# Kernel tuning notes

Measured on AMD Instinct MI355X. Metric: run time of the kernel, lower is better.

## Reference

```python
import jax, jax.numpy as jnp
import numpy as np

MUL = 64  # multiplicity of 0e and 1o in each input (irreps: 64x0e + 64x1o)
SQRT3 = float(np.sqrt(3.0))
SQRT2 = float(np.sqrt(2.0))
# Levi-Civita tensor: wigner_3j(1,1,1) is eps/sqrt(6); with 'component' norm it is scaled by sqrt(3) -> eps/sqrt(2)
_EPS = np.zeros((3, 3, 3), dtype=np.float32)
_EPS[0, 1, 2] = _EPS[1, 2, 0] = _EPS[2, 0, 1] = 1.0
_EPS[0, 2, 1] = _EPS[2, 1, 0] = _EPS[1, 0, 2] = -1.0
EPS = jnp.asarray(_EPS)


def setup_inputs() -> dict:
    key = jax.random.key(0)
    k1, k2 = jax.random.split(key)
    N = 4096
    D = MUL * (1 + 3)  # 64 scalars (0e) + 64 vectors (1o) = 256
    return {
        "input1": jax.random.normal(k1, (N, D), dtype=jnp.float32),
        "input2": jax.random.normal(k2, (N, D), dtype=jnp.float32),
    }


def _full_tensor_product(input1, input2):
    lead = input1.shape[:-1]
    a0 = input1[..., :MUL]                            # (..., 64)    0e chunk
    a1 = input1[..., MUL:].reshape(lead + (MUL, 3))   # (..., 64, 3) 1o chunk
    b0 = input2[..., :MUL]
    b1 = input2[..., MUL:].reshape(lead + (MUL, 3))
    # 'component' normalization: cg *= sqrt(dim(ir_out))
    # path 0e x 0e -> 0e : cg = 1
    c_000 = jnp.einsum('...u,...v->...uv', a0, b0).reshape(lead + (MUL * MUL,))
    # path 1o x 1o -> 0e : cg = eye(3)/sqrt(3)  (normalized dot product)
    c_110 = (jnp.einsum('...ui,...vi->...uv', a1, b1) / SQRT3).reshape(lead + (MUL * MUL,))
    # path 0e x 1o -> 1o : cg = eye(3)  (eye/sqrt3 * sqrt3)
    c_011 = jnp.einsum('...u,...vj->...uvj', a0, b1).reshape(lead + (MUL * MUL * 3,))
    # path 1o x 0e -> 1o : cg = eye(3)
    c_101 = jnp.einsum('...ui,...v->...uvi', a1, b0).reshape(lead + (MUL * MUL * 3,))
    # path 1o x 1o -> 1e : cg = eps/sqrt(2)  (normalized cross product)
    c_111 = jnp.einsum('...ui,...vj,ijk->...uvk', a1, b1, EPS / SQRT2).reshape(lead + (MUL * MUL * 3,))
    # sorted output irreps: 4096x0e + 4096x0e + 4096x1o + 4096x1o + 4096x1e
    # (inv = [0, 3, 1, 2, 4] over path-order chunks)
    return jnp.concatenate([c_000, c_110, c_011, c_101, c_111], axis=-1)


def reference(input1, input2):
    return _full_tensor_product(input1, input2)
```

## Files before the change

### kernel.cpp

```cpp
#include <hip/hip_runtime.h>


#define ROW_IN   256
#define ROW_OUT  45056

__global__ __launch_bounds__(256) void ftp_kernel(
    const float* __restrict__ in1,
    const float* __restrict__ in2,
    float* __restrict__ out)
{
    __shared__ float sa[ROW_IN];
    __shared__ float sb[ROW_IN];

    const int row = blockIdx.x;
    const int t   = threadIdx.x;

    sa[t] = in1[(size_t)row * ROW_IN + t];
    sb[t] = in2[(size_t)row * ROW_IN + t];
    __syncthreads();

    const float* a0 = sa;
    const float* a1 = sa + 64;
    const float* b0 = sb;
    const float* b1 = sb + 64;

    constexpr float INV_SQRT3 = 0.57735026918962576f;
    constexpr float INV_SQRT2 = 0.70710678118654752f;

    float4* __restrict__ outr = (float4*)(out + (size_t)row * ROW_OUT);

    #pragma unroll
    for (int it = 0; it < 4; ++it) {
        const int f = t + it * 256;
        const int e = f << 2;
        const int u = e >> 6;
        const int v = e & 63;
        const float au = a0[u];
        float4 r;
        r.x = au * b0[v + 0];
        r.y = au * b0[v + 1];
        r.z = au * b0[v + 2];
        r.w = au * b0[v + 3];
        outr[f] = r;
    }

    #pragma unroll
    for (int it = 0; it < 4; ++it) {
        const int f = t + it * 256;
        const int e = f << 2;
        const int u = e >> 6;
        const int v = e & 63;
        const float ax = a1[u * 3 + 0];
        const float ay = a1[u * 3 + 1];
        const float az = a1[u * 3 + 2];
        float4 r;
        {
            const float* bv = b1 + (v + 0) * 3;
            r.x = (ax * bv[0] + ay * bv[1] + az * bv[2]) * INV_SQRT3;
        }
        {
            const float* bv = b1 + (v + 1) * 3;
            r.y = (ax * bv[0] + ay * bv[1] + az * bv[2]) * INV_SQRT3;
        }
        {
            const float* bv = b1 + (v + 2) * 3;
            r.z = (ax * bv[0] + ay * bv[1] + az * bv[2]) * INV_SQRT3;
        }
        {
            const float* bv = b1 + (v + 3) * 3;
            r.w = (ax * bv[0] + ay * bv[1] + az * bv[2]) * INV_SQRT3;
        }
        outr[1024 + f] = r;
    }

    #pragma unroll
    for (int it = 0; it < 12; ++it) {
        const int f = t + it * 256;
        const int e = f << 2;
        const int u  = e / 192;
        const int r0 = e - u * 192;
        const float au = a0[u];
        float4 r;
        r.x = au * b1[r0 + 0];
        r.y = au * b1[r0 + 1];
        r.z = au * b1[r0 + 2];
        r.w = au * b1[r0 + 3];
        outr[2048 + f] = r;
    }

    #pragma unroll
    for (int it = 0; it < 12; ++it) {
        const int f = t + it * 256;
        const int e = f << 2;
        const int u  = e / 192;
        const int r0 = e - u * 192;
        const float* au = a1 + u * 3;
        float vals[4];
        #pragma unroll
        for (int j = 0; j < 4; ++j) {
            const int rr = r0 + j;
            const int v  = rr / 3;
            const int i  = rr - 3 * v;
            vals[j] = au[i] * b0[v];
        }
        float4 r;
        r.x = vals[0]; r.y = vals[1]; r.z = vals[2]; r.w = vals[3];
        outr[5120 + f] = r;
    }

    #pragma unroll
    for (int it = 0; it < 12; ++it) {
        const int f = t + it * 256;
        const int e = f << 2;
        const int u  = e / 192;
        const int r0 = e - u * 192;
        const float* au = a1 + u * 3;
        float vals[4];
        #pragma unroll
        for (int j = 0; j < 4; ++j) {
            const int rr = r0 + j;
            const int v  = rr / 3;
            const int k  = rr - 3 * v;
            const int k1 = (k < 2) ? k + 1 : 0;
            const int k2 = (k1 < 2) ? k1 + 1 : 0;
            const float* bv = b1 + v * 3;
            vals[j] = (au[k1] * bv[k2] - au[k2] * bv[k1]) * INV_SQRT2;
        }
        float4 r;
        r.x = vals[0]; r.y = vals[1]; r.z = vals[2]; r.w = vals[3];
        outr[8192 + f] = r;
    }
}

extern "C" void kernel_launch(void* const* d_in, const int* in_sizes, int n_in,
                              void* d_out, int out_size, void* d_ws, size_t ws_size,
                              hipStream_t stream) {
    const float* in1 = (const float*)d_in[0];
    const float* in2 = (const float*)d_in[1];
    float* out = (float*)d_out;
    const int N = in_sizes[0] / ROW_IN;
    ftp_kernel<<<N, 256, 0, stream>>>(in1, in2, out);
}
```

Baseline: 727.1 us.

## Split each row across four blocks and compute per-thread u,v tiles

Each output row is now handled by four blocks, each covering 16 values of u, and each thread computes every path for one (u, 4 consecutive v) tile from register-held inputs. This removes the per-element integer division and modulo and the repeated shared-memory gathers, and reuses the loaded a and b values across all five paths. In exchange, each row's inputs are loaded four times. Per-thread writes become three consecutive float4s, which changes the store coalescing pattern.

```diff
diff --git a/kernel.cpp b/kernel.cpp
--- a/kernel.cpp
+++ b/kernel.cpp
@@ -12,123 +12,100 @@
     __shared__ float sa[ROW_IN];
     __shared__ float sb[ROW_IN];
 
-    const int row = blockIdx.x;
+    const int bid = blockIdx.x;
+    const int row = bid >> 2;
+    const int jb  = bid & 3;
     const int t   = threadIdx.x;
 
     sa[t] = in1[(size_t)row * ROW_IN + t];
     sb[t] = in2[(size_t)row * ROW_IN + t];
     __syncthreads();
 
-    const float* a0 = sa;
-    const float* a1 = sa + 64;
-    const float* b0 = sb;
-    const float* b1 = sb + 64;
+    const int u  = (jb << 4) + (t >> 4);
+    const int vq = t & 15;
+    const int v  = vq << 2;
+
+    const float a0u = sa[u];
+    const float ax  = sa[64 + u * 3 + 0];
+    const float ay  = sa[64 + u * 3 + 1];
+    const float az  = sa[64 + u * 3 + 2];
+
+    const float4 b0v = *(const float4*)(sb + v);
+    const float4 q0  = *(const float4*)(sb + 64 + v * 3);
+    const float4 q1  = *(const float4*)(sb + 64 + v * 3 + 4);
+    const float4 q2  = *(const float4*)(sb + 64 + v * 3 + 8);
+
+    const float b1x0 = q0.x, b1y0 = q0.y, b1z0 = q0.z;
+    const float b1x1 = q0.w, b1y1 = q1.x, b1z1 = q1.y;
+    const float b1x2 = q1.z, b1y2 = q1.w, b1z2 = q2.x;
+    const float b1x3 = q2.y, b1y3 = q2.z, b1z3 = q2.w;
 
     constexpr float INV_SQRT3 = 0.57735026918962576f;
     constexpr float INV_SQRT2 = 0.70710678118654752f;
 
     float4* __restrict__ outr = (float4*)(out + (size_t)row * ROW_OUT);
 
-    #pragma unroll
-    for (int it = 0; it < 4; ++it) {
-        const int f = t + it * 256;
-        const int e = f << 2;
-        const int u = e >> 6;
-        const int v = e & 63;
-        const float au = a0[u];
+    const int f00   = u * 16 + vq;
+    const int base3 = u * 48 + vq * 3;
+
+    {
         float4 r;
-        r.x = au * b0[v + 0];
-        r.y = au * b0[v + 1];
-        r.z = au * b0[v + 2];
-        r.w = au * b0[v + 3];
-        outr[f] = r;
+        r.x = a0u * b0v.x;
+        r.y = a0u * b0v.y;
+        r.z = a0u * b0v.z;
+        r.w = a0u * b0v.w;
+        outr[f00] = r;
     }
 
-    #pragma unroll
-    for (int it = 0; it < 4; ++it) {
-        const int f = t + it * 256;
-        const int e = f << 2;
-        const int u = e >> 6;
-        const int v = e & 63;
-        const float ax = a1[u * 3 + 0];
-        const float ay = a1[u * 3 + 1];
-        const float az = a1[u * 3 + 2];
+    {
         float4 r;
-        {
-            const float* bv = b1 + (v + 0) * 3;
-            r.x = (ax * bv[0] + ay * bv[1] + az * bv[2]) * INV_SQRT3;
-        }
-        {
-            const float* bv = b1 + (v + 1) * 3;
-            r.y = (ax * bv[0] + ay * bv[1] + az * bv[2]) * INV_SQRT3;
-        }
-        {
-            const float* bv = b1 + (v + 2) * 3;
-            r.z = (ax * bv[0] + ay * bv[1] + az * bv[2]) * INV_SQRT3;
-        }
-        {
-            const float* bv = b1 + (v + 3) * 3;
-            r.w = (ax * bv[0] + ay * bv[1] + az * bv[2]) * INV_SQRT3;
-        }
-        outr[1024 + f] = r;
+        r.x = (ax * b1x0 + ay * b1y0 + az * b1z0) * INV_SQRT3;
+        r.y = (ax * b1x1 + ay * b1y1 + az * b1z1) * INV_SQRT3;
+        r.z = (ax * b1x2 + ay * b1y2 + az * b1z2) * INV_SQRT3;
+        r.w = (ax * b1x3 + ay * b1y3 + az * b1z3) * INV_SQRT3;
+        outr[1024 + f00] = r;
     }
 
-    #pragma unroll
-    for (int it = 0; it < 12; ++it) {
-        const int f = t + it * 256;
-        const int e = f << 2;
-        const int u  = e / 192;
-        const int r0 = e - u * 192;
-        const float au = a0[u];
-        float4 r;
-        r.x = au * b1[r0 + 0];
-        r.y = au * b1[r0 + 1];
-        r.z = au * b1[r0 + 2];
-        r.w = au * b1[r0 + 3];
-        outr[2048 + f] = r;
+    {
+        float4 r0, r1, r2;
+        r0.x = a0u * b1x0; r0.y = a0u * b1y0; r0.z = a0u * b1z0; r0.w = a0u * b1x1;
+        r1.x = a0u * b1y1; r1.y = a0u * b1z1; r1.z = a0u * b1x2; r1.w = a0u * b1y2;
+        r2.x = a0u * b1z2; r2.y = a0u * b1x3; r2.z = a0u * b1y3; r2.w = a0u * b1z3;
+        outr[2048 + base3 + 0] = r0;
+        outr[2048 + base3 + 1] = r1;
+        outr[2048 + base3 + 2] = r2;
     }
 
-    #pragma unroll
-    for (int it = 0; it < 12; ++it) {
-        const int f = t + it * 256;
-        const int e = f << 2;
-        const int u  = e / 192;
-        const int r0 = e - u * 192;
-        const float* au = a1 + u * 3;
-        float vals[4];
-        #pragma unroll
-        for (int j = 0; j < 4; ++j) {
-            const int rr = r0 + j;
-            const int v  = rr / 3;
-            const int i  = rr - 3 * v;
-            vals[j] = au[i] * b0[v];
-        }
-        float4 r;
-        r.x = vals[0]; r.y = vals[1]; r.z = vals[2]; r.w = vals[3];
-        outr[5120 + f] = r;
+    {
+        float4 r0, r1, r2;
+        r0.x = ax * b0v.x; r0.y = ay * b0v.x; r0.z = az * b0v.x; r0.w = ax * b0v.y;
+        r1.x = ay * b0v.y; r1.y = az * b0v.y; r1.z = ax * b0v.z; r1.w = ay * b0v.z;
+        r2.x = az * b0v.z; r2.y = ax * b0v.w; r2.z = ay * b0v.w; r2.w = az * b0v.w;
+        outr[5120 + base3 + 0] = r0;
+        outr[5120 + base3 + 1] = r1;
+        outr[5120 + base3 + 2] = r2;
     }
 
-    #pragma unroll
-    for (int it = 0; it < 12; ++it) {
-        const int f = t + it * 256;
-        const int e = f << 2;
-        const int u  = e / 192;
-        const int r0 = e - u * 192;
-        const float* au = a1 + u * 3;
-        float vals[4];
-        #pragma unroll
-        for (int j = 0; j < 4; ++j) {
-            const int rr = r0 + j;
-            const int v  = rr / 3;
-            const int k  = rr - 3 * v;
-            const int k1 = (k < 2) ? k + 1 : 0;
-            const int k2 = (k1 < 2) ? k1 + 1 : 0;
-            const float* bv = b1 + v * 3;
-            vals[j] = (au[k1] * bv[k2] - au[k2] * bv[k1]) * INV_SQRT2;
-        }
-        float4 r;
-        r.x = vals[0]; r.y = vals[1]; r.z = vals[2]; r.w = vals[3];
-        outr[8192 + f] = r;
+    {
+        const float c0x = (ay * b1z0 - az * b1y0) * INV_SQRT2;
+        const float c0y = (az * b1x0 - ax * b1z0) * INV_SQRT2;
+        const float c0z = (ax * b1y0 - ay * b1x0) * INV_SQRT2;
+        const float c1x = (ay * b1z1 - az * b1y1) * INV_SQRT2;
+        const float c1y = (az * b1x1 - ax * b1z1) * INV_SQRT2;
+        const float c1z = (ax * b1y1 - ay * b1x1) * INV_SQRT2;
+        const float c2x = (ay * b1z2 - az * b1y2) * INV_SQRT2;
+        const float c2y = (az * b1x2 - ax * b1z2) * INV_SQRT2;
+        const float c2z = (ax * b1y2 - ay * b1x2) * INV_SQRT2;
+        const float c3x = (ay * b1z3 - az * b1y3) * INV_SQRT2;
+        const float c3y = (az * b1x3 - ax * b1z3) * INV_SQRT2;
+        const float c3z = (ax * b1y3 - ay * b1x3) * INV_SQRT2;
+        float4 r0, r1, r2;
+        r0.x = c0x; r0.y = c0y; r0.z = c0z; r0.w = c1x;
+        r1.x = c1y; r1.y = c1z; r1.z = c2x; r1.w = c2y;
+        r2.x = c2z; r2.y = c3x; r2.z = c3y; r2.w = c3z;
+        outr[8192 + base3 + 0] = r0;
+        outr[8192 + base3 + 1] = r1;
+        outr[8192 + base3 + 2] = r2;
     }
 }
 
@@ -139,5 +116,5 @@
     const float* in2 = (const float*)d_in[1];
     float* out = (float*)d_out;
     const int N = in_sizes[0] / ROW_IN;
-    ftp_kernel<<<N, 256, 0, stream>>>(in1, in2, out);
+    ftp_kernel<<<(N * 4), 256, 0, stream>>>(in1, in2, out);
 }
```

After: 724.1 us. About the same (-0.4%).
